# Kernel optimization log

Measured on AMD Instinct MI355X. Metric: run time of the kernel, lower is better.

## Reference

```python
import jax, jax.numpy as jnp
import numpy as np

NUM_QUBITS = 4
QUANTUM_DEPTH = 2
BATCH = 1048576

# Hadamard matrix
_H = jnp.asarray(np.array([[1.0, 1.0], [1.0, -1.0]]) / np.sqrt(2.0), jnp.complex64)

# PauliZ sign table: signs[w, k] = +/-1 for basis state k on wire w (wire 0 = most significant axis)
_idx = np.arange(16)
_SIGNS = jnp.asarray(np.stack([1.0 - 2.0 * ((_idx >> (NUM_QUBITS - 1 - w)) & 1) for w in range(NUM_QUBITS)]), jnp.float32)  # (4,16)


def _apply_1q(state, U, w):
    # state: (B,2,2,2,2); apply 2x2 U on wire w
    a = 1 + w
    s = jnp.moveaxis(state, a, -1)
    s = s @ U.T  # new_j = sum_i U[j,i] * s[..., i]
    return jnp.moveaxis(s, -1, a)


def _apply_rz(state, theta, w):
    # diagonal RZ(theta) = diag(e^{-i t/2}, e^{i t/2}), theta: (B,)
    ph = jnp.exp(1j * jnp.stack([-theta / 2, theta / 2], axis=-1).astype(jnp.complex64))  # (B,2)
    shape = [state.shape[0], 1, 1, 1, 1]
    shape[1 + w] = 2
    return state * ph.reshape(shape)


def _cnot(state, c, t):
    ca, ta = 1 + c, 1 + t
    s0 = jnp.take(state, 0, axis=ca)
    s1 = jnp.take(state, 1, axis=ca)
    s1 = jnp.flip(s1, axis=ta if ta < ca else ta - 1)
    return jnp.stack([s0, s1], axis=ca)


def _ry_matrix(theta):
    c, s = jnp.cos(theta / 2), jnp.sin(theta / 2)
    return jnp.stack([jnp.stack([c, -s]), jnp.stack([s, c])]).astype(jnp.complex64)


def _simulate(inputs, params):
    B = inputs.shape[0]
    state = jnp.zeros((B, 2, 2, 2, 2), jnp.complex64).at[:, 0, 0, 0, 0].set(1.0)
    # feature map: H on all wires, RZ(inputs[:, w]), CNOT chain
    for w in range(NUM_QUBITS):
        state = _apply_1q(state, _H, w)
    for w in range(NUM_QUBITS):
        state = _apply_rz(state, inputs[:, w], w)
    for w in range(NUM_QUBITS - 1):
        state = _cnot(state, w, w + 1)
    # variational circuit
    for layer in range(QUANTUM_DEPTH):
        for w in range(NUM_QUBITS):
            state = _apply_1q(state, _ry_matrix(params[layer, w]), w)
        for w in range(NUM_QUBITS - 1):
            state = _cnot(state, w, w + 1)
        state = _cnot(state, NUM_QUBITS - 1, 0)
    probs = jnp.abs(state.reshape(B, 16)) ** 2  # (B,16) float32
    return probs @ _SIGNS.T  # (B,4) expvals of PauliZ per wire


def setup_inputs() -> dict:
    key = jax.random.key(0)
    k1, k2 = jax.random.split(key)
    inputs = jax.random.normal(k1, (BATCH, NUM_QUBITS), jnp.float32)
    params = jax.random.normal(k2, (QUANTUM_DEPTH, NUM_QUBITS), jnp.float32) * 0.1
    return {"inputs": inputs, "params": params}


def reference(inputs, params):
    return _simulate(inputs, params)
```

## Files before the change

kernel.cpp:

```cpp
#include <hip/hip_runtime.h>


typedef float v2f __attribute__((ext_vector_type(2)));

__global__ void qprep_kernel(const float* __restrict__ params, float* __restrict__ tab) {
    __shared__ float V[16][16];
    __shared__ float4 T[81];
    const int tid = threadIdx.x;
    if (tid < 81) T[tid] = make_float4(0.f, 0.f, 0.f, 0.f);
    if (tid < 16) {
        float col[16];
        #pragma unroll
        for (int j = 0; j < 16; ++j) col[j] = (j == tid) ? 1.f : 0.f;
        auto cnot = [&](int cm, int tm) {
            #pragma unroll
            for (int j = 0; j < 16; ++j)
                if ((j & cm) && !(j & tm)) { int k = j | tm; float t0 = col[j]; col[j] = col[k]; col[k] = t0; }
        };
        auto ry = [&](int m, float c, float s) {
            #pragma unroll
            for (int j = 0; j < 16; ++j)
                if (!(j & m)) { int k = j | m; float a0 = col[j], a1 = col[k]; col[j] = c*a0 - s*a1; col[k] = s*a0 + c*a1; }
        };
        cnot(8, 4); cnot(4, 2); cnot(2, 1);
        #pragma unroll
        for (int l = 0; l < 2; ++l) {
            float cp[4], sp[4];
            #pragma unroll
            for (int w = 0; w < 4; ++w) __sincosf(0.5f * params[l*4 + w], &sp[w], &cp[w]);
            ry(8, cp[0], sp[0]); ry(4, cp[1], sp[1]); ry(2, cp[2], sp[2]); ry(1, cp[3], sp[3]);
            cnot(8, 4); cnot(4, 2); cnot(2, 1); cnot(1, 8);
        }
        #pragma unroll
        for (int j = 0; j < 16; ++j) V[j][tid] = col[j];
    }
    __syncthreads();
    for (int it = tid; it < 1024; it += 256) {
        const int w = it >> 8, m = (it >> 4) & 15, mp = it & 15;
        if (m == mp) continue;
        int t = 0; int first = 1;
        #pragma unroll
        for (int u = 0; u < 4; ++u) {
            const int d = ((m >> (3 - u)) & 1) - ((mp >> (3 - u)) & 1) + 1;
            t = t * 3 + d;
            if (first == 1 && d != 1) first = d;
        }
        if (first != 2) continue;
        float g = 0.f;
        #pragma unroll
        for (int k = 0; k < 16; ++k) {
            const float sgn = ((k >> (3 - w)) & 1) ? -1.f : 1.f;
            g += sgn * V[k][m] * V[k][mp];
        }
        atomicAdd(((float*)&T[t]) + w, 0.125f * g);
    }
    __syncthreads();
    if (tid < 81) reinterpret_cast<float4*>(tab)[tid] = T[tid];
}

__device__ __forceinline__ v2f cm2(v2f a, v2f bv, v2f br) { return a.x * bv + a.y * br; }

__global__ __launch_bounds__(256) void qmain_kernel(
    const float* __restrict__ inputs,
    const float4* __restrict__ tab,
    float* __restrict__ out,
    int B)
{
    const int b = blockIdx.x * blockDim.x + threadIdx.x;
    if (b >= B) return;
    const float4 x = reinterpret_cast<const float4*>(inputs)[b];

    v2f e[4], r[4], ec[4], rc[4];
    {
        float cc, ss;
        __sincosf(x.x, &ss, &cc); e[0] = (v2f){cc, ss};
        __sincosf(x.y, &ss, &cc); e[1] = (v2f){cc, ss};
        __sincosf(x.z, &ss, &cc); e[2] = (v2f){cc, ss};
        __sincosf(x.w, &ss, &cc); e[3] = (v2f){cc, ss};
    }
    #pragma unroll
    for (int u = 0; u < 4; ++u) {
        r[u]  = (v2f){-e[u].y, e[u].x};
        ec[u] = (v2f){ e[u].x, -e[u].y};
        rc[u] = (v2f){ e[u].y,  e[u].x};
    }

    v2f P2[9], P3[27];
    #pragma unroll
    for (int t = 0; t < 9; ++t) {
        const int d0 = t / 3, d1 = t % 3;
        if (d0 == 0 || (d0 == 1 && d1 == 0)) continue;
        if (d0 == 1) P2[t] = (d1 == 1) ? (v2f){1.f, 0.f} : e[1];
        else         P2[t] = (d1 == 1) ? e[0]
                           : (d1 == 2) ? cm2(e[0], e[1], r[1])
                                       : cm2(e[0], ec[1], rc[1]);
    }
    #pragma unroll
    for (int t = 0; t < 27; ++t) {
        const int d0 = t / 9, d1 = (t / 3) % 3, d2 = t % 3;
        const bool ones01 = (d0 == 1 && d1 == 1);
        if (d0 == 0 || (d0 == 1 && d1 == 0) || (ones01 && d2 == 0)) continue;
        if (ones01) P3[t] = (d2 == 1) ? (v2f){1.f, 0.f} : e[2];
        else {
            const int tp = t / 3;
            P3[t] = (d2 == 1) ? P2[tp]
                  : (d2 == 2) ? cm2(P2[tp], e[2], r[2])
                              : cm2(P2[tp], ec[2], rc[2]);
        }
    }

    v2f o01 = (v2f){0.f, 0.f}, o23 = (v2f){0.f, 0.f};
    #pragma unroll
    for (int t = 0; t < 81; ++t) {
        const int d0 = t / 27, d1 = (t / 9) % 3, d2 = (t / 3) % 3, d3 = t % 3;
        const int first = (d0 != 1) ? d0 : (d1 != 1) ? d1 : (d2 != 1) ? d2 : (d3 != 1) ? d3 : 1;
        if (first != 2) continue;
        const bool ones012 = (d0 == 1 && d1 == 1 && d2 == 1);
        float cv;
        if (ones012) cv = e[3].x;
        else {
            const int tp = t / 3;
            if (d3 == 1)      cv = P3[tp].x;
            else if (d3 == 2) cv = P3[tp].x * e[3].x - P3[tp].y * e[3].y;
            else              cv = P3[tp].x * e[3].x + P3[tp].y * e[3].y;
        }
        const float4 cf = tab[t];
        o01 += cv * (v2f){cf.x, cf.y};
        o23 += cv * (v2f){cf.z, cf.w};
    }

    reinterpret_cast<float4*>(out)[b] = make_float4(o01.x, o01.y, o23.x, o23.y);
}

extern "C" void kernel_launch(void* const* d_in, const int* in_sizes, int n_in,
                              void* d_out, int out_size, void* d_ws, size_t ws_size,
                              hipStream_t stream) {
    const float* inputs = (const float*)d_in[0];
    const float* params = (const float*)d_in[1];
    float* out = (float*)d_out;
    float* tab = (float*)d_ws;
    const int B = in_sizes[0] / 4;

    qprep_kernel<<<1, 256, 0, stream>>>(params, tab);
    const int threads = 256;
    const int blocks = (B + threads - 1) / threads;
    qmain_kernel<<<blocks, threads, 0, stream>>>(inputs, (const float4*)tab, out, B);
}
```

Before: 75.54 us.

## Fuse coefficient-table prep into main kernel with per-block shuffle-based unitary build

Drops the separate single-block prep kernel. Each block now rebuilds the 16x16 circuit unitary itself, with 256 threads each holding one matrix element and applying the gates through wavefront shuffles. It then reduces the 81-entry coefficient table into shared memory and reads it from there instead of from global memory. This removes one kernel launch and the serial dependency between the two kernels, at the cost of repeating the prep work, including shared-memory atomics and two barriers, in all 4096 blocks.

```diff
diff --git a/kernel.cpp b/kernel.cpp
--- a/kernel.cpp
+++ b/kernel.cpp
@@ -3,24 +3,33 @@
 
 typedef float v2f __attribute__((ext_vector_type(2)));
 
-__global__ void qprep_kernel(const float* __restrict__ params, float* __restrict__ tab) {
-    __shared__ float V[16][16];
+__device__ __forceinline__ v2f cm2(v2f a, v2f bv, v2f br) { return a.x * bv + a.y * br; }
+
+__global__ __launch_bounds__(256) void qfused_kernel(
+    const float* __restrict__ inputs,
+    const float* __restrict__ params,
+    float* __restrict__ out,
+    int B)
+{
+    __shared__ float Vs[16][17];
     __shared__ float4 T[81];
+
     const int tid = threadIdx.x;
-    if (tid < 81) T[tid] = make_float4(0.f, 0.f, 0.f, 0.f);
-    if (tid < 16) {
-        float col[16];
-        #pragma unroll
-        for (int j = 0; j < 16; ++j) col[j] = (j == tid) ? 1.f : 0.f;
+    const int b = blockIdx.x * blockDim.x + tid;
+
+    float4 x;
+    if (b < B) x = reinterpret_cast<const float4*>(inputs)[b];
+
+    {
+        const int c = tid >> 4, r = tid & 15;
+        float A = (r == c) ? 1.f : 0.f;
         auto cnot = [&](int cm, int tm) {
-            #pragma unroll
-            for (int j = 0; j < 16; ++j)
-                if ((j & cm) && !(j & tm)) { int k = j | tm; float t0 = col[j]; col[j] = col[k]; col[k] = t0; }
+            float P = __shfl_xor(A, tm);
+            A = (r & cm) ? P : A;
         };
-        auto ry = [&](int m, float c, float s) {
-            #pragma unroll
-            for (int j = 0; j < 16; ++j)
-                if (!(j & m)) { int k = j | m; float a0 = col[j], a1 = col[k]; col[j] = c*a0 - s*a1; col[k] = s*a0 + c*a1; }
+        auto ry = [&](int m, float cp, float sp) {
+            float P = __shfl_xor(A, m);
+            A = cp * A + sp * ((r & m) ? P : -P);
         };
         cnot(8, 4); cnot(4, 2); cnot(2, 1);
         #pragma unroll
@@ -31,10 +40,11 @@
             ry(8, cp[0], sp[0]); ry(4, cp[1], sp[1]); ry(2, cp[2], sp[2]); ry(1, cp[3], sp[3]);
             cnot(8, 4); cnot(4, 2); cnot(2, 1); cnot(1, 8);
         }
-        #pragma unroll
-        for (int j = 0; j < 16; ++j) V[j][tid] = col[j];
+        Vs[c][r] = A;
+        if (tid < 81) T[tid] = make_float4(0.f, 0.f, 0.f, 0.f);
     }
     __syncthreads();
+
     for (int it = tid; it < 1024; it += 256) {
         const int w = it >> 8, m = (it >> 4) & 15, mp = it & 15;
         if (m == mp) continue;
@@ -50,25 +60,13 @@
         #pragma unroll
         for (int k = 0; k < 16; ++k) {
             const float sgn = ((k >> (3 - w)) & 1) ? -1.f : 1.f;
-            g += sgn * V[k][m] * V[k][mp];
+            g += sgn * Vs[m][k] * Vs[mp][k];
         }
         atomicAdd(((float*)&T[t]) + w, 0.125f * g);
     }
     __syncthreads();
-    if (tid < 81) reinterpret_cast<float4*>(tab)[tid] = T[tid];
-}
 
-__device__ __forceinline__ v2f cm2(v2f a, v2f bv, v2f br) { return a.x * bv + a.y * br; }
-
-__global__ __launch_bounds__(256) void qmain_kernel(
-    const float* __restrict__ inputs,
-    const float4* __restrict__ tab,
-    float* __restrict__ out,
-    int B)
-{
-    const int b = blockIdx.x * blockDim.x + threadIdx.x;
     if (b >= B) return;
-    const float4 x = reinterpret_cast<const float4*>(inputs)[b];
 
     v2f e[4], r[4], ec[4], rc[4];
     {
@@ -124,7 +122,7 @@
             else if (d3 == 2) cv = P3[tp].x * e[3].x - P3[tp].y * e[3].y;
             else              cv = P3[tp].x * e[3].x + P3[tp].y * e[3].y;
         }
-        const float4 cf = tab[t];
+        const float4 cf = T[t];
         o01 += cv * (v2f){cf.x, cf.y};
         o23 += cv * (v2f){cf.z, cf.w};
     }
@@ -138,11 +136,9 @@
     const float* inputs = (const float*)d_in[0];
     const float* params = (const float*)d_in[1];
     float* out = (float*)d_out;
-    float* tab = (float*)d_ws;
     const int B = in_sizes[0] / 4;
 
-    qprep_kernel<<<1, 256, 0, stream>>>(params, tab);
     const int threads = 256;
     const int blocks = (B + threads - 1) / threads;
-    qmain_kernel<<<blocks, threads, 0, stream>>>(inputs, (const float4*)tab, out, B);
+    qfused_kernel<<<blocks, threads, 0, stream>>>(inputs, params, out, B);
 }
```

After: 92.74 us. 1.23x slower.
